# Performance work log

Hardware: AMD Instinct MI355X
Metric: run time of the kernel (lower is better)

The kernel has to match this reference:

```python
import jax, jax.numpy as jnp
import numpy as np

B, S, D = 32, 512, 1024  # batch, seq_len, input_dim == output_dim


def setup_inputs() -> dict:
    key = jax.random.key(0)
    ks = jax.random.split(key, 13)
    std = 0.05  # tf.random_normal_initializer default stddev
    w = lambda k, shp: (jax.random.normal(k, shp, dtype=jnp.float32) * std)
    inp = {"seq_input_vec": jax.random.normal(ks[0], (B, S, D), dtype=jnp.float32)}
    names = ["Ui", "Wi", "Uf", "Wf", "Uo", "Wo", "Ug", "Wg"]
    for i, n in enumerate(names):
        inp[n] = w(ks[1 + i], (D, D))
    for n in ["bi", "bf", "bo", "bg"]:
        inp[n] = jnp.zeros((D,), dtype=jnp.float32)
    return inp


def reference(seq_input_vec, Ui, Wi, bi, Uf, Wf, bf, Uo, Wo, bo, Ug, Wg, bg):
    # seq_input_vec: [B, S, D]. Fuse the 4 input projections into one GEMM
    # over the whole sequence (mathematically identical to per-step matmuls).
    U = jnp.concatenate([Ui, Uf, Uo, Ug], axis=1)          # [D, 4D]
    W = jnp.concatenate([Wi, Wf, Wo, Wg], axis=1)          # [D, 4D]
    b = jnp.concatenate([bi, bf, bo, bg], axis=0)          # [4D]
    x_proj = jnp.einsum('bsd,de->sbe', seq_input_vec, U) + b  # [S, B, 4D]

    d = seq_input_vec.shape[-1]
    h0 = jnp.zeros((seq_input_vec.shape[0], d), dtype=seq_input_vec.dtype)
    c0 = jnp.zeros_like(h0)

    def step(carry, xp):
        c_prev, h_prev = carry
        z = xp + h_prev @ W                                 # [B, 4D]
        zi, zf, zo, zg = jnp.split(z, 4, axis=-1)
        i_t = jax.nn.sigmoid(zi)
        f_t = jax.nn.sigmoid(zf)
        o_t = jax.nn.sigmoid(zo)
        g_t = jnp.tanh(zg)
        # NOTE: original (nonstandard) math applies sigmoid to the cell update
        c_t = jax.nn.sigmoid(f_t * c_prev + i_t * g_t)
        h_t = jnp.tanh(c_t) * o_t
        return (c_t, h_t), h_t

    _, hs = jax.lax.scan(step, (c0, h0), x_proj)            # hs: [S, B, D]
    return jnp.transpose(hs, (1, 0, 2))                     # [B, S, D]
```

## Files before the change

kernel.cpp:

```cpp
#include <hip/hip_runtime.h>

typedef unsigned int u32;
typedef unsigned short u16;
typedef unsigned long long u64;
typedef __attribute__((ext_vector_type(8))) short short8;
typedef __attribute__((ext_vector_type(4))) float f32x4;

#define SEQ 512
#define BATCH 32
#define DIM 1024
#define NB 128

#define OFF_XT    0ull
#define OFF_UBT   33554432ull
#define OFF_WG2   41943040ull
#define OFF_XPROJ 50331648ull
#define OFF_HBUF  184549376ull
#define OFF_BIAS  184680448ull
#define OFF_SYNC  184696832ull

__device__ __forceinline__ float bf2f(u16 u) {
  union { u32 u; float f; } v; v.u = ((u32)u) << 16; return v.f;
}
__device__ __forceinline__ u16 f2bf(float f) {
  union { float f; u32 u; } v; v.f = f;
  u32 r = v.u + 0x7FFFu + ((v.u >> 16) & 1u);
  return (u16)(r >> 16);
}
__device__ __forceinline__ void gload_lds16(const u16* g, u16* l) {
  __builtin_amdgcn_global_load_lds(
      (const __attribute__((address_space(1))) u32*)g,
      (__attribute__((address_space(3))) u32*)l, 16, 0, 0);
}
__device__ __forceinline__ void gload_lds16_coh(const u16* g, u16* l) {
  __builtin_amdgcn_global_load_lds(
      (const __attribute__((address_space(1))) u32*)g,
      (__attribute__((address_space(3))) u32*)l, 16, 0, 17);
}

__global__ void k_init(u32* hb, float* biasc, u32* sync,
                       const float* bi, const float* bfv,
                       const float* bo, const float* bg) {
  int i = blockIdx.x * 256 + threadIdx.x;
  if (i < 32768) {
    hb[i] = 0u;
  } else if (i < 32768 + 4096) {
    int e = i - 32768;
    int g = e >> 10, c = e & 1023;
    const float* p = (g == 0) ? bi : (g == 1) ? bfv : (g == 2) ? bo : bg;
    biasc[e] = p[c];
  } else if (i < 32768 + 4096 + 4096) {
    sync[i - 32768 - 4096] = 0u;
  }
}

__global__ void k_prep_w(const float* Ui, const float* Wi, const float* Uf,
                         const float* Wf, const float* Uo, const float* Wo,
                         const float* Ug, const float* Wg, u16* Ubt, u16* Wg2) {
  __shared__ float tile[64][65];
  int bx = blockIdx.x;
  int mi = bx >> 8;
  int tt = bx & 255;
  int tr = tt >> 4, tc = tt & 15;
  const float* src;
  switch (mi) {
    case 0: src = Ui; break; case 1: src = Wi; break;
    case 2: src = Uf; break; case 3: src = Wf; break;
    case 4: src = Uo; break; case 5: src = Wo; break;
    case 6: src = Ug; break; default: src = Wg; break;
  }
  int g = mi >> 1;
  int d0 = tr * 64, c0 = tc * 64;
  int ty = threadIdx.x >> 6, tx = threadIdx.x & 63;
#pragma unroll
  for (int i = 0; i < 16; ++i) {
    int r = i * 4 + ty;
    tile[r][tx] = src[(size_t)(d0 + r) * 1024 + c0 + tx];
  }
  __syncthreads();
  if (mi & 1) {
#pragma unroll
    for (int i = 0; i < 16; ++i) {
      int cc = i * 4 + ty;
      int c_full = c0 + cc;
      int k = d0 + tx;
      int blk = c_full >> 3;
      int rr = (g << 3) | (c_full & 7);
      Wg2[(size_t)blk * 32768 + ((k >> 5) << 10) + rr * 32 + (k & 31)] =
          f2bf(tile[tx][cc]);
    }
  } else {
#pragma unroll
    for (int i = 0; i < 16; ++i) {
      int cc = i * 4 + ty;
      Ubt[(size_t)((g << 10) + c0 + cc) * 1024 + d0 + tx] = f2bf(tile[tx][cc]);
    }
  }
}

__global__ void k_prep_x(const float* __restrict__ X, u16* __restrict__ Xt) {
  int idx = blockIdx.x * 256 + threadIdx.x;
  int m = idx >> 8, d4 = (idx & 255) << 2;
  int s = m >> 5, b = m & 31;
  const float4* p = (const float4*)(X + (size_t)(b * SEQ + s) * DIM + d4);
  float4 v = *p;
  u16 o[4] = { f2bf(v.x), f2bf(v.y), f2bf(v.z), f2bf(v.w) };
  *(ushort4*)(Xt + (size_t)m * DIM + d4) = *(ushort4*)o;
}

__global__ __launch_bounds__(256) void k_gemm(const u16* __restrict__ Xt,
                                              const u16* __restrict__ Ubt,
                                              const float* __restrict__ biasc,
                                              u16* __restrict__ xproj) {
  __shared__ u16 As[128 * 32];
  __shared__ u16 Bs[128 * 32];
  int tid = threadIdx.x;
  int w = tid >> 6, l = tid & 63;
  int n0 = blockIdx.x * 128, m0 = blockIdx.y * 128;
  int wm = w >> 1, wn = w & 1;
  int lrow = l & 15, lq = l >> 4;
  f32x4 acc[4][4] = {};
  for (int kt = 0; kt < 32; ++kt) {
    int k0 = kt * 32;
    __syncthreads();
#pragma unroll
    for (int is = 0; is < 2; ++is) {
      int c = is * 256 + w * 64 + l;
      int row = c >> 2, kg = c & 3;
      gload_lds16(Xt + (size_t)(m0 + row) * 1024 + k0 + kg * 8, As + c * 8);
      gload_lds16(Ubt + (size_t)(n0 + row) * 1024 + k0 + kg * 8, Bs + c * 8);
    }
    __syncthreads();
    short8 af[4], bf[4];
#pragma unroll
    for (int mt = 0; mt < 4; ++mt)
      af[mt] = *(const short8*)(As + (wm * 64 + mt * 16 + lrow) * 32 + lq * 8);
#pragma unroll
    for (int nt = 0; nt < 4; ++nt)
      bf[nt] = *(const short8*)(Bs + (wn * 64 + nt * 16 + lrow) * 32 + lq * 8);
#pragma unroll
    for (int mt = 0; mt < 4; ++mt)
#pragma unroll
      for (int nt = 0; nt < 4; ++nt)
        acc[mt][nt] = __builtin_amdgcn_mfma_f32_16x16x32_bf16(
            af[mt], bf[nt], acc[mt][nt], 0, 0, 0);
  }
#pragma unroll
  for (int nt = 0; nt < 4; ++nt) {
    int col = n0 + wn * 64 + nt * 16 + lrow;
    float bv = biasc[col];
#pragma unroll
    for (int mt = 0; mt < 4; ++mt) {
      int rbase = m0 + wm * 64 + mt * 16 + lq * 4;
#pragma unroll
      for (int r = 0; r < 4; ++r)
        xproj[(size_t)(rbase + r) * 4096 + col] = f2bf(acc[mt][nt][r] + bv);
    }
  }
}

__global__ __launch_bounds__(256, 1) void k_rec(const u16* __restrict__ Wg2,
                                                const u16* __restrict__ xproj,
                                                u16* hbuf, float* out, u32* sync) {
  __shared__ u16 Ws[32 * 1024];
  __shared__ u16 Hs[32 * 1024];
  __shared__ u16 XPs[32 * 32];
  __shared__ float zbuf[32][33];
  int tid = threadIdx.x;
  int w = tid >> 6, l = tid & 63;
  int blk = blockIdx.x;
  int lrow = l & 15, lq = l >> 4;
#pragma unroll
  for (int it = 0; it < 16; ++it) {
    int c = it * 256 + w * 64 + l;
    gload_lds16(Wg2 + (size_t)blk * 32768 + c * 8, Ws + c * 8);
  }
  if (w < 2) {
    int c2 = w * 64 + l;
    int b = c2 >> 2, g = c2 & 3;
    gload_lds16(xproj + (size_t)b * 4096 + (g << 10) + (blk << 3), XPs + c2 * 8);
  }
  float c_reg = 0.f;
  int eb = tid >> 3, ec = tid & 7;
  int mt = w >> 1, nt = w & 1;
  const u16* ap0 = Hs + (mt * 16 + lrow) * 32 + lq * 8;
  const u16* bp0 = Ws + (nt * 16 + lrow) * 32 + lq * 8;
  u16* hst_base = hbuf + ((blk >> 2) << 10) + eb * 32 + ((blk & 3) << 3) + ec;
  float* out_base = out + (size_t)eb * SEQ * DIM + (blk << 3) + ec;
  __syncthreads();

  for (int s = 0; s < SEQ; ++s) {
    const u16* hsrc = hbuf + (size_t)(s & 1) * 32768;
#pragma unroll
    for (int it = 0; it < 16; ++it) {
      int c = it * 256 + w * 64 + l;
      gload_lds16_coh(hsrc + c * 8, Hs + c * 8);
    }
    __syncthreads();

    f32x4 acc0 = { 0.f, 0.f, 0.f, 0.f };
    f32x4 acc1 = { 0.f, 0.f, 0.f, 0.f };
#pragma unroll
    for (int ks = 0; ks < 16; ++ks) {
      short8 a0 = *(const short8*)(ap0 + (2 * ks) * 1024);
      short8 b0 = *(const short8*)(bp0 + (2 * ks) * 1024);
      short8 a1 = *(const short8*)(ap0 + (2 * ks + 1) * 1024);
      short8 b1 = *(const short8*)(bp0 + (2 * ks + 1) * 1024);
      acc0 = __builtin_amdgcn_mfma_f32_16x16x32_bf16(a0, b0, acc0, 0, 0, 0);
      acc1 = __builtin_amdgcn_mfma_f32_16x16x32_bf16(a1, b1, acc1, 0, 0, 0);
    }
    f32x4 acc = acc0 + acc1;
    {
      int col = nt * 16 + lrow;
      int rb = mt * 16 + lq * 4;
#pragma unroll
      for (int r = 0; r < 4; ++r) zbuf[rb + r][col] = acc[r];
    }
    __syncthreads();

    float zi = zbuf[eb][ec]      + bf2f(XPs[eb * 32 + ec]);
    float zf = zbuf[eb][8 + ec]  + bf2f(XPs[eb * 32 + 8 + ec]);
    float zo = zbuf[eb][16 + ec] + bf2f(XPs[eb * 32 + 16 + ec]);
    float zg = zbuf[eb][24 + ec] + bf2f(XPs[eb * 32 + 24 + ec]);
    float ig = 1.f / (1.f + __expf(-zi));
    float fg = 1.f / (1.f + __expf(-zf));
    float og = 1.f / (1.f + __expf(-zo));
    float gg = tanhf(zg);
    c_reg = 1.f / (1.f + __expf(-(fg * c_reg + ig * gg)));
    float h = tanhf(c_reg) * og;
    __hip_atomic_store(hst_base + (size_t)(((s + 1) & 1)) * 32768, f2bf(h),
                       __ATOMIC_RELAXED, __HIP_MEMORY_SCOPE_AGENT);
    __syncthreads();

    if (tid == 0)
      __hip_atomic_store(sync + blk * 32, (u32)(s + 1), __ATOMIC_RELAXED,
                         __HIP_MEMORY_SCOPE_AGENT);
    {
      int sp = (s + 1 < SEQ) ? s + 1 : s;
      if (w < 2) {
        int c2 = w * 64 + l;
        int b = c2 >> 2, g = c2 & 3;
        gload_lds16(xproj + (size_t)(sp * 32 + b) * 4096 + (g << 10) + (blk << 3),
                    XPs + c2 * 8);
      }
    }
    __builtin_nontemporal_store(h, out_base + (size_t)s * DIM);

    if (w == 0) {
      u32 tgt = (u32)(s + 1);
      int guard = 0;
      for (;;) {
        u32 a = __hip_atomic_load(sync + l * 32, __ATOMIC_RELAXED,
                                  __HIP_MEMORY_SCOPE_AGENT);
        u32 b = __hip_atomic_load(sync + (64 + l) * 32, __ATOMIC_RELAXED,
                                  __HIP_MEMORY_SCOPE_AGENT);
        if (a >= tgt && b >= tgt) break;
        __builtin_amdgcn_s_sleep(1);
        if (++guard > 20000000) break;
      }
    }
    asm volatile("" ::: "memory");
    __syncthreads();
  }
}

extern "C" void kernel_launch(void* const* d_in, const int* in_sizes, int n_in,
                              void* d_out, int out_size, void* d_ws,
                              size_t ws_size, hipStream_t stream) {
  const float* X   = (const float*)d_in[0];
  const float* Ui  = (const float*)d_in[1];
  const float* Wi  = (const float*)d_in[2];
  const float* Uf  = (const float*)d_in[3];
  const float* Wf  = (const float*)d_in[4];
  const float* Uo  = (const float*)d_in[5];
  const float* Wo  = (const float*)d_in[6];
  const float* Ug  = (const float*)d_in[7];
  const float* Wg  = (const float*)d_in[8];
  const float* bi  = (const float*)d_in[9];
  const float* bfv = (const float*)d_in[10];
  const float* bo  = (const float*)d_in[11];
  const float* bg  = (const float*)d_in[12];
  char* ws = (char*)d_ws;
  u16* Xt      = (u16*)(ws + OFF_XT);
  u16* Ubt     = (u16*)(ws + OFF_UBT);
  u16* Wg2     = (u16*)(ws + OFF_WG2);
  u16* xproj   = (u16*)(ws + OFF_XPROJ);
  u16* hbuf    = (u16*)(ws + OFF_HBUF);
  float* biasc = (float*)(ws + OFF_BIAS);
  u32* sync    = (u32*)(ws + OFF_SYNC);
  float* out   = (float*)d_out;

  k_init<<<160, 256, 0, stream>>>((u32*)hbuf, biasc, sync, bi, bfv, bo, bg);
  k_prep_w<<<2048, 256, 0, stream>>>(Ui, Wi, Uf, Wf, Uo, Wo, Ug, Wg, Ubt, Wg2);
  k_prep_x<<<16384, 256, 0, stream>>>(X, Xt);
  k_gemm<<<dim3(32, 128), 256, 0, stream>>>(Xt, Ubt, biasc, xproj);
  k_rec<<<NB, 256, 0, stream>>>(Wg2, xproj, hbuf, out, sync);
}
```

Baseline: 1.961 ms.

## Replace global barrier with step-tagged hidden-state words polled per element

The recurrent kernel drops the separate sync flags and the grid-wide spin barrier. Each hidden value is now stored as a 32-bit word holding the step number in the high half and the bf16 value in the low half, and consumers poll their own loaded data until every tag matches the current step. The aim is to remove the extra barrier round-trip and the per-step __syncthreads, so blocks wait only on the data they actually need. In exchange, each step's hidden-state read doubles in size and is done with coherent register loads instead of direct-to-LDS loads. tanhf is also replaced with an exp-based fast tanh, and the hidden buffer reuses the Xt workspace region, which is zeroed after the GEMM.

```diff
diff --git a/kernel.cpp b/kernel.cpp
--- a/kernel.cpp
+++ b/kernel.cpp
@@ -5,6 +5,8 @@
 typedef unsigned long long u64;
 typedef __attribute__((ext_vector_type(8))) short short8;
 typedef __attribute__((ext_vector_type(4))) float f32x4;
+typedef __attribute__((ext_vector_type(4))) u32 u32x4;
+typedef __attribute__((ext_vector_type(2))) u32 u32x2;
 
 #define SEQ 512
 #define BATCH 32
@@ -15,9 +17,7 @@
 #define OFF_UBT   33554432ull
 #define OFF_WG2   41943040ull
 #define OFF_XPROJ 50331648ull
-#define OFF_HBUF  184549376ull
 #define OFF_BIAS  184680448ull
-#define OFF_SYNC  184696832ull
 
 __device__ __forceinline__ float bf2f(u16 u) {
   union { u32 u; float f; } v; v.u = ((u32)u) << 16; return v.f;
@@ -27,31 +27,27 @@
   u32 r = v.u + 0x7FFFu + ((v.u >> 16) & 1u);
   return (u16)(r >> 16);
 }
+__device__ __forceinline__ float tanh_fast(float x) {
+  return 1.f - 2.f / (1.f + __expf(2.f * x));
+}
 __device__ __forceinline__ void gload_lds16(const u16* g, u16* l) {
   __builtin_amdgcn_global_load_lds(
       (const __attribute__((address_space(1))) u32*)g,
       (__attribute__((address_space(3))) u32*)l, 16, 0, 0);
 }
-__device__ __forceinline__ void gload_lds16_coh(const u16* g, u16* l) {
-  __builtin_amdgcn_global_load_lds(
-      (const __attribute__((address_space(1))) u32*)g,
-      (__attribute__((address_space(3))) u32*)l, 16, 0, 17);
-}
-
-__global__ void k_init(u32* hb, float* biasc, u32* sync,
-                       const float* bi, const float* bfv,
+
+__global__ void k_init(float* biasc, const float* bi, const float* bfv,
                        const float* bo, const float* bg) {
-  int i = blockIdx.x * 256 + threadIdx.x;
-  if (i < 32768) {
-    hb[i] = 0u;
-  } else if (i < 32768 + 4096) {
-    int e = i - 32768;
+  int e = blockIdx.x * 256 + threadIdx.x;
+  if (e < 4096) {
     int g = e >> 10, c = e & 1023;
     const float* p = (g == 0) ? bi : (g == 1) ? bfv : (g == 2) ? bo : bg;
     biasc[e] = p[c];
-  } else if (i < 32768 + 4096 + 4096) {
-    sync[i - 32768 - 4096] = 0u;
-  }
+  }
+}
+
+__global__ void k_zero(u32x4* p) {
+  p[blockIdx.x * 256 + threadIdx.x] = (u32x4){0u, 0u, 0u, 0u};
 }
 
 __global__ void k_prep_w(const float* Ui, const float* Wi, const float* Uf,
@@ -131,19 +127,19 @@
       gload_lds16(Ubt + (size_t)(n0 + row) * 1024 + k0 + kg * 8, Bs + c * 8);
     }
     __syncthreads();
-    short8 af[4], bf[4];
+    short8 af[4], bfr[4];
 #pragma unroll
     for (int mt = 0; mt < 4; ++mt)
       af[mt] = *(const short8*)(As + (wm * 64 + mt * 16 + lrow) * 32 + lq * 8);
 #pragma unroll
     for (int nt = 0; nt < 4; ++nt)
-      bf[nt] = *(const short8*)(Bs + (wn * 64 + nt * 16 + lrow) * 32 + lq * 8);
+      bfr[nt] = *(const short8*)(Bs + (wn * 64 + nt * 16 + lrow) * 32 + lq * 8);
 #pragma unroll
     for (int mt = 0; mt < 4; ++mt)
 #pragma unroll
       for (int nt = 0; nt < 4; ++nt)
         acc[mt][nt] = __builtin_amdgcn_mfma_f32_16x16x32_bf16(
-            af[mt], bf[nt], acc[mt][nt], 0, 0, 0);
+            af[mt], bfr[nt], acc[mt][nt], 0, 0, 0);
   }
 #pragma unroll
   for (int nt = 0; nt < 4; ++nt) {
@@ -161,7 +157,7 @@
 
 __global__ __launch_bounds__(256, 1) void k_rec(const u16* __restrict__ Wg2,
                                                 const u16* __restrict__ xproj,
-                                                u16* hbuf, float* out, u32* sync) {
+                                                u32* hbt, float* out) {
   __shared__ u16 Ws[32 * 1024];
   __shared__ u16 Hs[32 * 1024];
   __shared__ u16 XPs[32 * 32];
@@ -185,16 +181,45 @@
   int mt = w >> 1, nt = w & 1;
   const u16* ap0 = Hs + (mt * 16 + lrow) * 32 + lq * 8;
   const u16* bp0 = Ws + (nt * 16 + lrow) * 32 + lq * 8;
-  u16* hst_base = hbuf + ((blk >> 2) << 10) + eb * 32 + ((blk & 3) << 3) + ec;
+  u32* hst = hbt + ((blk >> 2) << 10) + eb * 32 + ((blk & 3) << 3) + ec;
   float* out_base = out + (size_t)eb * SEQ * DIM + (blk << 3) + ec;
   __syncthreads();
 
   for (int s = 0; s < SEQ; ++s) {
-    const u16* hsrc = hbuf + (size_t)(s & 1) * 32768;
-#pragma unroll
-    for (int it = 0; it < 16; ++it) {
-      int c = it * 256 + w * 64 + l;
-      gload_lds16_coh(hsrc + c * 8, Hs + c * 8);
+    const u32* hsrc = hbt + (size_t)(s & 1) * 32768;
+    u32 T = (u32)s << 16;
+
+    u32x4 q[32];
+#pragma unroll
+    for (int qd = 0; qd < 32; ++qd) {
+      asm volatile("global_load_dwordx4 %0, %1, off sc0 sc1"
+                   : "=v"(q[qd])
+                   : "v"(hsrc + qd * 1024 + tid * 4));
+    }
+    asm volatile("s_waitcnt vmcnt(0)" ::: "memory");
+    __builtin_amdgcn_sched_barrier(0);
+
+#pragma unroll
+    for (int qd = 0; qd < 32; ++qd) {
+      const u32* p = hsrc + qd * 1024 + tid * 4;
+      int guard = 0;
+      for (;;) {
+        u32 m = (q[qd].x ^ T) | (q[qd].y ^ T) | (q[qd].z ^ T) | (q[qd].w ^ T);
+        if (!(m & 0xFFFF0000u)) break;
+        if (++guard > 20000000) break;
+        q[qd].x = __hip_atomic_load(p + 0, __ATOMIC_RELAXED,
+                                    __HIP_MEMORY_SCOPE_AGENT);
+        q[qd].y = __hip_atomic_load(p + 1, __ATOMIC_RELAXED,
+                                    __HIP_MEMORY_SCOPE_AGENT);
+        q[qd].z = __hip_atomic_load(p + 2, __ATOMIC_RELAXED,
+                                    __HIP_MEMORY_SCOPE_AGENT);
+        q[qd].w = __hip_atomic_load(p + 3, __ATOMIC_RELAXED,
+                                    __HIP_MEMORY_SCOPE_AGENT);
+      }
+      u32 p0 = __builtin_amdgcn_perm(q[qd].y, q[qd].x, 0x05040100u);
+      u32 p1 = __builtin_amdgcn_perm(q[qd].w, q[qd].z, 0x05040100u);
+      u32x2 pk = { p0, p1 };
+      *(u32x2*)((char*)Hs + qd * 2048 + tid * 8) = pk;
     }
     __syncthreads();
 
@@ -225,16 +250,14 @@
     float ig = 1.f / (1.f + __expf(-zi));
     float fg = 1.f / (1.f + __expf(-zf));
     float og = 1.f / (1.f + __expf(-zo));
-    float gg = tanhf(zg);
+    float gg = tanh_fast(zg);
     c_reg = 1.f / (1.f + __expf(-(fg * c_reg + ig * gg)));
-    float h = tanhf(c_reg) * og;
-    __hip_atomic_store(hst_base + (size_t)(((s + 1) & 1)) * 32768, f2bf(h),
+    float h = tanh_fast(c_reg) * og;
+
+    u32 hw = ((u32)(s + 1) << 16) | (u32)f2bf(h);
+    __hip_atomic_store(hst + (size_t)((s + 1) & 1) * 32768, hw,
                        __ATOMIC_RELAXED, __HIP_MEMORY_SCOPE_AGENT);
-    __syncthreads();
-
-    if (tid == 0)
-      __hip_atomic_store(sync + blk * 32, (u32)(s + 1), __ATOMIC_RELAXED,
-                         __HIP_MEMORY_SCOPE_AGENT);
+
     {
       int sp = (s + 1 < SEQ) ? s + 1 : s;
       if (w < 2) {
@@ -245,22 +268,6 @@
       }
     }
     __builtin_nontemporal_store(h, out_base + (size_t)s * DIM);
-
-    if (w == 0) {
-      u32 tgt = (u32)(s + 1);
-      int guard = 0;
-      for (;;) {
-        u32 a = __hip_atomic_load(sync + l * 32, __ATOMIC_RELAXED,
-                                  __HIP_MEMORY_SCOPE_AGENT);
-        u32 b = __hip_atomic_load(sync + (64 + l) * 32, __ATOMIC_RELAXED,
-                                  __HIP_MEMORY_SCOPE_AGENT);
-        if (a >= tgt && b >= tgt) break;
-        __builtin_amdgcn_s_sleep(1);
-        if (++guard > 20000000) break;
-      }
-    }
-    asm volatile("" ::: "memory");
-    __syncthreads();
   }
 }
 
@@ -282,17 +289,17 @@
   const float* bg  = (const float*)d_in[12];
   char* ws = (char*)d_ws;
   u16* Xt      = (u16*)(ws + OFF_XT);
+  u32* hbt     = (u32*)(ws + OFF_XT);
   u16* Ubt     = (u16*)(ws + OFF_UBT);
   u16* Wg2     = (u16*)(ws + OFF_WG2);
   u16* xproj   = (u16*)(ws + OFF_XPROJ);
-  u16* hbuf    = (u16*)(ws + OFF_HBUF);
   float* biasc = (float*)(ws + OFF_BIAS);
-  u32* sync    = (u32*)(ws + OFF_SYNC);
   float* out   = (float*)d_out;
 
-  k_init<<<160, 256, 0, stream>>>((u32*)hbuf, biasc, sync, bi, bfv, bo, bg);
+  k_init<<<16, 256, 0, stream>>>(biasc, bi, bfv, bo, bg);
   k_prep_w<<<2048, 256, 0, stream>>>(Ui, Wi, Uf, Wf, Uo, Wo, Ug, Wg, Ubt, Wg2);
   k_prep_x<<<16384, 256, 0, stream>>>(X, Xt);
   k_gemm<<<dim3(32, 128), 256, 0, stream>>>(Xt, Ubt, biasc, xproj);
-  k_rec<<<NB, 256, 0, stream>>>(Wg2, xproj, hbuf, out, sync);
-}
+  k_zero<<<64, 256, 0, stream>>>((u32x4*)hbt);
+  k_rec<<<NB, 256, 0, stream>>>(Wg2, xproj, hbt, out);
+}
```

After: 7.729 ms. 3.94x slower.
